# Kernel optimization log

Measured on AMD Instinct MI355X. Metric: run time of the kernel, lower is better.

## Reference

```python
import jax, jax.numpy as jnp
import numpy as np

B = 4      # cfg.TRAIN.IMS_PER_BATCH
P = 256    # proposals per image (equal per image; all labels > 0)
C = 151    # cfg.MODEL.NUM_CLASSES
R = 51     # cfg.MODEL.NUM_RELATIONS
W = 0.5    # cfg.REL_INFER.NONE_BGREL_WEIGHT


def setup_inputs() -> dict:
    key = jax.random.key(0)
    k1, k2, k3, k4 = jax.random.split(key, 4)
    roi_scores = jax.random.normal(k1, (B * P, C), dtype=jnp.float32)
    rel_scores = jax.random.normal(k2, (B * P * P, R), dtype=jnp.float32)
    roi_labels = jax.random.randint(k3, (B * P,), 1, C, dtype=jnp.int32)  # labels > 0 (fg only)
    # sparse relation co-occurrence matrix densified; background relation slice set to 1
    relationship_mat = (jax.random.uniform(k4, (C, C, R)) < 0.05).astype(jnp.float32)
    relationship_mat = relationship_mat.at[:, :, 0].set(1.0)
    return {
        "roi_scores": roi_scores,
        "rel_scores": rel_scores,
        "relationship_mat": relationship_mat,
        "roi_labels": roi_labels,
        "num_images": B,
    }


def reference(roi_scores, rel_scores, relationship_mat, roi_labels, num_images):
    nb = num_images
    p = roi_scores.shape[0] // nb
    rel = rel_scores.reshape(nb, p, p, -1)          # [B, P, P, R]
    labels = roi_labels.reshape(nb, p)              # [B, P]
    # computed in the original forward but unused by the returned loss
    _unary = jax.nn.log_softmax(roi_scores, axis=1)
    off_diag = (1.0 - jnp.eye(p, dtype=roi_scores.dtype))  # zero out p == q pairs

    def per_image(lab, rl):
        # lab: [P] int, rl: [P, P, R]
        A = relationship_mat[lab]        # [P, C, R]  rows gathered by subject label
        At = relationship_mat[:, lab]    # [C, P, R]  cols gathered by subject label
        # b[p,q,c] = A[p,c,0]*rl[p,q,0] + W * sum_{r>=1} A[p,c,r]*rl[p,q,r]
        b = A[:, None, :, 0] * rl[:, :, None, 0] \
            + W * jnp.einsum('pcr,pqr->pqc', A[..., 1:], rl[..., 1:])
        # t[p,q,c] = At[c,p,0]*rl[q,p,0] + W * sum_{r>=1} At[c,p,r]*rl[q,p,r]
        t = At[..., 0].T[:, None, :] * rl[..., 0].T[:, :, None] \
            + W * jnp.einsum('cpr,qpr->pqc', At[..., 1:], rl[..., 1:])
        theta = 0.5 * (b + t) * off_diag[:, :, None]  # mask diagonal pairs
        theta = theta.sum(0)                          # sum over partner p -> [P, C]
        logp = jax.nn.log_softmax(theta, axis=1)
        return -logp[jnp.arange(p), lab]              # [P]

    loss = jax.vmap(per_image)(labels, rel)           # [B, P]
    return loss.mean()
```

## Files before the change

### kernel.cpp

```cpp
#include <hip/hip_runtime.h>
#include <math.h>

#define NB 4
#define PP 256
#define CC 151
#define RR 51
#define CM 160
#define KI 64
#define KS 64
#define NROW (NB*PP)
#define RELTOT (NB*PP*PP*RR)
#define ALIM (RELTOT - 8)
#define MLB 10240

typedef _Float16 half8 __attribute__((ext_vector_type(8)));
typedef float floatx16 __attribute__((ext_vector_type(16)));

#define OFF_M1 ((size_t)0)
#define OFF_M2 (OFF_M1 + (size_t)CC*MLB*2)
#define OFF_PT (OFF_M2 + (size_t)CC*MLB*2)

__global__ __launch_bounds__(256) void prep_kernel(const float* __restrict__ M,
                                                   _Float16* __restrict__ m1,
                                                   _Float16* __restrict__ m2,
                                                   float* __restrict__ out) {
    const int l = blockIdx.x;
    const int mat = blockIdx.y;
    if (l == 0 && mat == 0 && threadIdx.x == 0) *out = 0.f;
    _Float16* dst = (mat ? m2 : m1) + (size_t)l * MLB;
    for (int e = threadIdx.x; e < MLB; e += 256) {
        int oct = e / 1280;
        int rem = e - oct * 1280;
        int c = rem >> 3, j = rem & 7;
        int r = oct * 8 + j;
        float v = 0.f;
        if (r < RR && c < CC) {
            size_t src = ((size_t)(mat ? c * CC + l : l * CC + c)) * RR + r;
            v = (r == 0 ? 0.5f : 0.25f) * M[src];
        }
        dst[e] = (_Float16)v;
    }
}

__global__ __launch_bounds__(256) void gemm_kernel(const float* __restrict__ rel,
                                                   const _Float16* __restrict__ m1,
                                                   const _Float16* __restrict__ m2,
                                                   const int* __restrict__ labels,
                                                   float* __restrict__ part) {
    __shared__ _Float16 Bt[2][2560];
    const int tid  = threadIdx.x;
    const int ks   = blockIdx.x & 63;
    const int rbk  = (blockIdx.x >> 6) & 1;
    const int n    = blockIdx.x >> 7;
    const int wave = tid >> 6, lane = tid & 63;
    const int m32  = lane & 31, kh = lane >> 5;
    const int i0   = ks * 4;
    const int rowimg = rbk * 128 + wave * 32 + m32;

    int labs[4];
    #pragma unroll
    for (int j = 0; j < 4; ++j) labs[j] = labels[n * PP + i0 + j];

    floatx16 acc[5];
    #pragma unroll
    for (int ct = 0; ct < 5; ++ct)
        #pragma unroll
        for (int r2 = 0; r2 < 16; ++r2) acc[ct][r2] = 0.f;

    auto stageB = [&](int h, int buf) {
        const int il = h >> 3, mh = (h >> 2) & 1, t = h & 3;
        const _Float16* base = (mh ? m2 : m1) + (size_t)labs[il] * MLB + t * 2560;
        #pragma unroll
        for (int j = 0; j < 2; ++j) {
            int s = j * 256 + tid;
            if (s < 320) {
                __builtin_amdgcn_global_load_lds(
                    (const __attribute__((address_space(1))) unsigned int*)(base + s * 8),
                    (__attribute__((address_space(3))) unsigned int*)(&Bt[buf][(size_t)s * 8]),
                    16, 0, 0);
            }
        }
    };
    auto loadA = [&](int h, float* v) {
        const int il = h >> 3, mh = (h >> 2) & 1, t = h & 3;
        const int i = i0 + il;
        const int r0 = t * 16 + kh * 8;
        int idx = mh ? ((n * PP + rowimg) * PP + i) * RR + r0
                     : ((n * PP + i) * PP + rowimg) * RR + r0;
        idx = min(idx, ALIM);
        const float* p = rel + idx;
        #pragma unroll
        for (int j = 0; j < 8; ++j) v[j] = p[j];
    };

    stageB(0, 0);
    float av[8];
    loadA(0, av);

    #pragma unroll 2
    for (int h = 0; h < 32; ++h) {
        __syncthreads();
        if (h < 31) stageB(h + 1, (h + 1) & 1);
        float avn[8];
        if (h < 31) loadA(h + 1, avn);

        const bool dz = (i0 + (h >> 3)) == rowimg;
        half8 a;
        #pragma unroll
        for (int j = 0; j < 8; ++j) a[j] = (_Float16)(dz ? 0.f : av[j]);

        const _Float16* bb = &Bt[h & 1][(size_t)(kh * 160 + m32) * 8];
        #pragma unroll
        for (int ct = 0; ct < 5; ++ct) {
            half8 b = *(const half8*)(bb + ct * 256);
            acc[ct] = __builtin_amdgcn_mfma_f32_32x32x16_f16(a, b, acc[ct], 0, 0, 0);
        }
        #pragma unroll
        for (int j = 0; j < 8; ++j) av[j] = avn[j];
    }

    float* pb = part + ((size_t)ks * NROW + n * PP + rbk * 128 + wave * 32) * CM;
    #pragma unroll
    for (int ct = 0; ct < 5; ++ct)
        #pragma unroll
        for (int reg = 0; reg < 16; ++reg) {
            int row = (reg & 3) + 8 * (reg >> 2) + 4 * kh;
            pb[(size_t)row * CM + ct * 32 + m32] = acc[ct][reg];
        }
}

__global__ __launch_bounds__(256) void reduce_loss_kernel(const float* __restrict__ part,
                                                          const int* __restrict__ labels,
                                                          float* __restrict__ out) {
    __shared__ float th[CM];
    const int row = blockIdx.x;
    const int t = threadIdx.x;
    if (t < CM) {
        float s = 0.f;
        #pragma unroll
        for (int ks = 0; ks < KS; ++ks)
            s += part[((size_t)ks * NROW + row) * CM + t];
        th[t] = s;
    }
    __syncthreads();
    if (t < 64) {
        float v0 = (t < CC)       ? th[t]       : -INFINITY;
        float v1 = (t + 64 < CC)  ? th[t + 64]  : -INFINITY;
        float v2 = (t + 128 < CC) ? th[t + 128] : -INFINITY;
        float m = fmaxf(v0, fmaxf(v1, v2));
        #pragma unroll
        for (int o = 32; o > 0; o >>= 1) m = fmaxf(m, __shfl_xor(m, o, 64));
        float s = 0.f;
        if (t < CC)       s += expf(v0 - m);
        if (t + 64 < CC)  s += expf(v1 - m);
        if (t + 128 < CC) s += expf(v2 - m);
        #pragma unroll
        for (int o = 32; o > 0; o >>= 1) s += __shfl_xor(s, o, 64);
        if (t == 0) {
            atomicAdd(out, (m + logf(s) - th[labels[row]]) * (1.0f / NROW));
        }
    }
}

extern "C" void kernel_launch(void* const* d_in, const int* in_sizes, int n_in,
                              void* d_out, int out_size, void* d_ws, size_t ws_size,
                              hipStream_t stream) {
    const float* rel    = (const float*)d_in[1];
    const float* relmat = (const float*)d_in[2];
    const int*   labels = (const int*)d_in[3];
    float* out = (float*)d_out;
    char* ws = (char*)d_ws;

    _Float16* m1 = (_Float16*)(ws + OFF_M1);
    _Float16* m2 = (_Float16*)(ws + OFF_M2);
    float*  part = (float*)(ws + OFF_PT);

    prep_kernel<<<dim3(CC, 2), 256, 0, stream>>>(relmat, m1, m2, out);
    gemm_kernel<<<NB * 2 * KS, 256, 0, stream>>>(rel, m1, m2, labels, part);
    reduce_loss_kernel<<<NROW, 256, 0, stream>>>(part, labels, out);
}
```

Baseline: 166.6 us.

## Stage rel tiles through LDS with async loads and 4-deep pipeline

The A operand (rel scores) is now loaded with global_load_lds directly into a swizzled LDS buffer instead of into registers. The B operand staging is reorganized to two loads per thread. Both go into a 4-buffer ring with two steps of prefetch, gated by manual vmcnt waits and barriers. This aims to hide global load latency behind the MFMA work and cut register pressure. The cost is many 4-byte async loads per step and fragile hand-counted waitcnt values.

```diff
diff --git a/kernel.cpp b/kernel.cpp
--- a/kernel.cpp
+++ b/kernel.cpp
@@ -6,15 +6,14 @@
 #define CC 151
 #define RR 51
 #define CM 160
-#define KI 64
 #define KS 64
 #define NROW (NB*PP)
 #define RELTOT (NB*PP*PP*RR)
-#define ALIM (RELTOT - 8)
 #define MLB 10240
 
 typedef _Float16 half8 __attribute__((ext_vector_type(8)));
 typedef float floatx16 __attribute__((ext_vector_type(16)));
+typedef float float4v __attribute__((ext_vector_type(4)));
 
 #define OFF_M1 ((size_t)0)
 #define OFF_M2 (OFF_M1 + (size_t)CC*MLB*2)
@@ -47,7 +46,8 @@
                                                    const _Float16* __restrict__ m2,
                                                    const int* __restrict__ labels,
                                                    float* __restrict__ part) {
-    __shared__ _Float16 Bt[2][2560];
+    __shared__ float    ldsA[4][2048];
+    __shared__ _Float16 ldsB[4][2560];
     const int tid  = threadIdx.x;
     const int ks   = blockIdx.x & 63;
     const int rbk  = (blockIdx.x >> 6) & 1;
@@ -55,11 +55,18 @@
     const int wave = tid >> 6, lane = tid & 63;
     const int m32  = lane & 31, kh = lane >> 5;
     const int i0   = ks * 4;
-    const int rowimg = rbk * 128 + wave * 32 + m32;
+    const int row_loc = wave * 32 + m32;
+    const int rowimg  = rbk * 128 + row_loc;
 
-    int labs[4];
-    #pragma unroll
-    for (int j = 0; j < 4; ++j) labs[j] = labels[n * PP + i0 + j];
+    const int l0 = labels[n * PP + i0 + 0];
+    const int l1 = labels[n * PP + i0 + 1];
+    const int l2 = labels[n * PP + i0 + 2];
+    const int l3 = labels[n * PP + i0 + 3];
+
+    const int s_swz = (row_loc >> 1) & 3;
+    const int pA    = (2 * kh) ^ s_swz;
+    const int aoffL = row_loc * 16 + pA * 4;
+    const int aoffH = row_loc * 16 + (pA ^ 1) * 4;
 
     floatx16 acc[5];
     #pragma unroll
@@ -67,56 +74,67 @@
         #pragma unroll
         for (int r2 = 0; r2 < 16; ++r2) acc[ct][r2] = 0.f;
 
-    auto stageB = [&](int h, int buf) {
+    auto issueStep = [&](int h, int buf) {
         const int il = h >> 3, mh = (h >> 2) & 1, t = h & 3;
-        const _Float16* base = (mh ? m2 : m1) + (size_t)labs[il] * MLB + t * 2560;
+        const int i = i0 + il;
+        const int lab = (il & 2) ? ((il & 1) ? l3 : l2) : ((il & 1) ? l1 : l0);
+        const _Float16* mb = (mh ? m2 : m1) + (size_t)lab * MLB + t * 2560;
+        __builtin_amdgcn_global_load_lds(
+            (const __attribute__((address_space(1))) unsigned int*)(mb + tid * 8),
+            (__attribute__((address_space(3))) unsigned int*)(&ldsB[buf][tid * 8]),
+            16, 0, 0);
+        __builtin_amdgcn_global_load_lds(
+            (const __attribute__((address_space(1))) unsigned int*)(mb + 2048 + tid * 2),
+            (__attribute__((address_space(3))) unsigned int*)(&ldsB[buf][2048 + tid * 2]),
+            4, 0, 0);
         #pragma unroll
-        for (int j = 0; j < 2; ++j) {
-            int s = j * 256 + tid;
-            if (s < 320) {
-                __builtin_amdgcn_global_load_lds(
-                    (const __attribute__((address_space(1))) unsigned int*)(base + s * 8),
-                    (__attribute__((address_space(3))) unsigned int*)(&Bt[buf][(size_t)s * 8]),
-                    16, 0, 0);
-            }
+        for (int jj = 0; jj < 8; ++jj) {
+            const int tau = jj * 256 + tid;
+            const int row = tau >> 4;
+            const int q   = (tau >> 2) & 3;
+            const int e   = tau & 3;
+            const int ql  = q ^ ((row >> 1) & 3);
+            const int rg  = rbk * 128 + row;
+            int f = (mh ? ((n * PP + rg) * PP + i)
+                        : ((n * PP + i) * PP + rg)) * RR + t * 16 + ql * 4 + e;
+            f = min(f, RELTOT - 1);
+            __builtin_amdgcn_global_load_lds(
+                (const __attribute__((address_space(1))) unsigned int*)(rel + f),
+                (__attribute__((address_space(3))) unsigned int*)(&ldsA[buf][tau]),
+                4, 0, 0);
         }
     };
-    auto loadA = [&](int h, float* v) {
-        const int il = h >> 3, mh = (h >> 2) & 1, t = h & 3;
-        const int i = i0 + il;
-        const int r0 = t * 16 + kh * 8;
-        int idx = mh ? ((n * PP + rowimg) * PP + i) * RR + r0
-                     : ((n * PP + i) * PP + rowimg) * RR + r0;
-        idx = min(idx, ALIM);
-        const float* p = rel + idx;
-        #pragma unroll
-        for (int j = 0; j < 8; ++j) v[j] = p[j];
-    };
 
-    stageB(0, 0);
-    float av[8];
-    loadA(0, av);
-
-    #pragma unroll 2
-    for (int h = 0; h < 32; ++h) {
-        __syncthreads();
-        if (h < 31) stageB(h + 1, (h + 1) & 1);
-        float avn[8];
-        if (h < 31) loadA(h + 1, avn);
-
-        const bool dz = (i0 + (h >> 3)) == rowimg;
+    auto computeStep = [&](int h, int buf) {
+        const int il = h >> 3;
+        const bool dz = (i0 + il) == rowimg;
+        const float4v alo = *(const float4v*)(&ldsA[buf][aoffL]);
+        const float4v ahi = *(const float4v*)(&ldsA[buf][aoffH]);
         half8 a;
         #pragma unroll
-        for (int j = 0; j < 8; ++j) a[j] = (_Float16)(dz ? 0.f : av[j]);
-
-        const _Float16* bb = &Bt[h & 1][(size_t)(kh * 160 + m32) * 8];
+        for (int j = 0; j < 4; ++j) {
+            a[j]     = (_Float16)(dz ? 0.f : alo[j]);
+            a[j + 4] = (_Float16)(dz ? 0.f : ahi[j]);
+        }
+        const _Float16* bb = &ldsB[buf][(kh * 160 + m32) * 8];
         #pragma unroll
         for (int ct = 0; ct < 5; ++ct) {
             half8 b = *(const half8*)(bb + ct * 256);
             acc[ct] = __builtin_amdgcn_mfma_f32_32x32x16_f16(a, b, acc[ct], 0, 0, 0);
         }
-        #pragma unroll
-        for (int j = 0; j < 8; ++j) av[j] = avn[j];
+    };
+
+    issueStep(0, 0);
+    issueStep(1, 1);
+
+    for (int h = 0; h < 32; ++h) {
+        if (h < 30) issueStep(h + 2, (h + 2) & 3);
+        if (h < 30)       asm volatile("s_waitcnt vmcnt(20)" ::: "memory");
+        else if (h == 30) asm volatile("s_waitcnt vmcnt(10)" ::: "memory");
+        else              asm volatile("s_waitcnt vmcnt(0)"  ::: "memory");
+        __builtin_amdgcn_s_barrier();
+        asm volatile("" ::: "memory");
+        computeStep(h, h & 3);
     }
 
     float* pb = part + ((size_t)ks * NROW + n * PP + rbk * 128 + wave * 32) * CM;
```

Result: slower. 232.5 us (+39.5%).

## Load B operand directly into registers and drop LDS staging and barriers

Applied to the files above, without the earlier changes.

The GEMM kernel no longer stages the relation-matrix tile into shared memory through global_load_lds with a barrier each step. Each lane now loads its B fragments straight from global memory into registers, using a fully unrolled two-deep register double buffer for both A and B. Launch bounds now request two blocks per SM. This removes the per-step __syncthreads and the LDS round trip, but each wave issues its own redundant B loads and register pressure rises.

```diff
diff --git a/kernel.cpp b/kernel.cpp
--- a/kernel.cpp
+++ b/kernel.cpp
@@ -6,7 +6,6 @@
 #define CC 151
 #define RR 51
 #define CM 160
-#define KI 64
 #define KS 64
 #define NROW (NB*PP)
 #define RELTOT (NB*PP*PP*RR)
@@ -42,12 +41,11 @@
     }
 }
 
-__global__ __launch_bounds__(256) void gemm_kernel(const float* __restrict__ rel,
-                                                   const _Float16* __restrict__ m1,
-                                                   const _Float16* __restrict__ m2,
-                                                   const int* __restrict__ labels,
-                                                   float* __restrict__ part) {
-    __shared__ _Float16 Bt[2][2560];
+__global__ __launch_bounds__(256, 2) void gemm_kernel(const float* __restrict__ rel,
+                                                      const _Float16* __restrict__ m1,
+                                                      const _Float16* __restrict__ m2,
+                                                      const int* __restrict__ labels,
+                                                      float* __restrict__ part) {
     const int tid  = threadIdx.x;
     const int ks   = blockIdx.x & 63;
     const int rbk  = (blockIdx.x >> 6) & 1;
@@ -67,20 +65,6 @@
         #pragma unroll
         for (int r2 = 0; r2 < 16; ++r2) acc[ct][r2] = 0.f;
 
-    auto stageB = [&](int h, int buf) {
-        const int il = h >> 3, mh = (h >> 2) & 1, t = h & 3;
-        const _Float16* base = (mh ? m2 : m1) + (size_t)labs[il] * MLB + t * 2560;
-        #pragma unroll
-        for (int j = 0; j < 2; ++j) {
-            int s = j * 256 + tid;
-            if (s < 320) {
-                __builtin_amdgcn_global_load_lds(
-                    (const __attribute__((address_space(1))) unsigned int*)(base + s * 8),
-                    (__attribute__((address_space(3))) unsigned int*)(&Bt[buf][(size_t)s * 8]),
-                    16, 0, 0);
-            }
-        }
-    };
     auto loadA = [&](int h, float* v) {
         const int il = h >> 3, mh = (h >> 2) & 1, t = h & 3;
         const int i = i0 + il;
@@ -92,31 +76,35 @@
         #pragma unroll
         for (int j = 0; j < 8; ++j) v[j] = p[j];
     };
-
-    stageB(0, 0);
-    float av[8];
-    loadA(0, av);
-
-    #pragma unroll 2
-    for (int h = 0; h < 32; ++h) {
-        __syncthreads();
-        if (h < 31) stageB(h + 1, (h + 1) & 1);
-        float avn[8];
-        if (h < 31) loadA(h + 1, avn);
-
-        const bool dz = (i0 + (h >> 3)) == rowimg;
+    auto loadB = [&](int h, half8* b) {
+        const int il = h >> 3, mh = (h >> 2) & 1, t = h & 3;
+        const _Float16* p = (mh ? m2 : m1) + (size_t)labs[il] * MLB + t * 2560
+                          + (size_t)(kh * 160 + m32) * 8;
+        #pragma unroll
+        for (int ct = 0; ct < 5; ++ct) b[ct] = *(const half8*)(p + ct * 256);
+    };
+    auto computeStep = [&](int h, const float* av, const half8* bv) {
+        const int il = h >> 3;
+        const bool dz = (i0 + il) == rowimg;
         half8 a;
         #pragma unroll
         for (int j = 0; j < 8; ++j) a[j] = (_Float16)(dz ? 0.f : av[j]);
+        #pragma unroll
+        for (int ct = 0; ct < 5; ++ct)
+            acc[ct] = __builtin_amdgcn_mfma_f32_32x32x16_f16(a, bv[ct], acc[ct], 0, 0, 0);
+    };
 
-        const _Float16* bb = &Bt[h & 1][(size_t)(kh * 160 + m32) * 8];
-        #pragma unroll
-        for (int ct = 0; ct < 5; ++ct) {
-            half8 b = *(const half8*)(bb + ct * 256);
-            acc[ct] = __builtin_amdgcn_mfma_f32_32x32x16_f16(a, b, acc[ct], 0, 0, 0);
-        }
-        #pragma unroll
-        for (int j = 0; j < 8; ++j) av[j] = avn[j];
+    float aA[8], aB[8];
+    half8 bA[5], bB[5];
+    loadA(0, aA); loadB(0, bA);
+    loadA(1, aB); loadB(1, bB);
+
+    #pragma unroll
+    for (int h = 0; h < 32; h += 2) {
+        computeStep(h, aA, bA);
+        if (h + 2 < 32) { loadA(h + 2, aA); loadB(h + 2, bA); }
+        computeStep(h + 1, aB, bB);
+        if (h + 3 < 32) { loadA(h + 3, aB); loadB(h + 3, bB); }
     }
 
     float* pb = part + ((size_t)ks * NROW + n * PP + rbk * 128 + wave * 32) * CM;
```

Measured after the change: 173.1 us. 3.9% more time.

## Pre-convert relation scores to padded fp16 rows with diagonal zeroed

Applied to the files above, without the earlier changes.

Adds a pass inside the prep kernel that converts the fp32 relation-score tensor into fp16 rows padded to 64 entries, zeroing diagonal pairs and the padding. The GEMM kernel then loads eight halves per lane with one aligned vector load, instead of eight scalar fp32 loads followed by conversion and a diagonal check. This swaps strided unaligned fp32 reads in the GEMM for one extra full pass over the ~53MB rel tensor plus a ~33MB fp16 write, which may cost more bandwidth than it saves.

```diff
diff --git a/kernel.cpp b/kernel.cpp
--- a/kernel.cpp
+++ b/kernel.cpp
@@ -6,43 +6,65 @@
 #define CC 151
 #define RR 51
 #define CM 160
-#define KI 64
 #define KS 64
 #define NROW (NB*PP)
-#define RELTOT (NB*PP*PP*RR)
-#define ALIM (RELTOT - 8)
 #define MLB 10240
+#define NRELROW (NB*PP*PP)
+#define CONVB (NRELROW/8)
+#define PREPB (CC*2)
 
 typedef _Float16 half8 __attribute__((ext_vector_type(8)));
+typedef _Float16 half2v __attribute__((ext_vector_type(2)));
 typedef float floatx16 __attribute__((ext_vector_type(16)));
 
 #define OFF_M1 ((size_t)0)
 #define OFF_M2 (OFF_M1 + (size_t)CC*MLB*2)
 #define OFF_PT (OFF_M2 + (size_t)CC*MLB*2)
+#define OFF_R16 (OFF_PT + (size_t)KS*NROW*CM*4)
 
 __global__ __launch_bounds__(256) void prep_kernel(const float* __restrict__ M,
+                                                   const float* __restrict__ rel,
                                                    _Float16* __restrict__ m1,
                                                    _Float16* __restrict__ m2,
+                                                   _Float16* __restrict__ rel16,
                                                    float* __restrict__ out) {
-    const int l = blockIdx.x;
-    const int mat = blockIdx.y;
-    if (l == 0 && mat == 0 && threadIdx.x == 0) *out = 0.f;
-    _Float16* dst = (mat ? m2 : m1) + (size_t)l * MLB;
-    for (int e = threadIdx.x; e < MLB; e += 256) {
-        int oct = e / 1280;
-        int rem = e - oct * 1280;
-        int c = rem >> 3, j = rem & 7;
-        int r = oct * 8 + j;
-        float v = 0.f;
-        if (r < RR && c < CC) {
-            size_t src = ((size_t)(mat ? c * CC + l : l * CC + c)) * RR + r;
-            v = (r == 0 ? 0.5f : 0.25f) * M[src];
+    const int bid = blockIdx.x;
+    if (bid < PREPB) {
+        const int l = (bid < CC) ? bid : bid - CC;
+        const int mat = (bid < CC) ? 0 : 1;
+        if (bid == 0 && threadIdx.x == 0) *out = 0.f;
+        _Float16* dst = (mat ? m2 : m1) + (size_t)l * MLB;
+        for (int e = threadIdx.x; e < MLB; e += 256) {
+            int oct = e / 1280;
+            int rem = e - oct * 1280;
+            int c = rem >> 3, j = rem & 7;
+            int r = oct * 8 + j;
+            float v = 0.f;
+            if (r < RR && c < CC) {
+                size_t src = ((size_t)(mat ? c * CC + l : l * CC + c)) * RR + r;
+                v = (r == 0 ? 0.5f : 0.25f) * M[src];
+            }
+            dst[e] = (_Float16)v;
         }
-        dst[e] = (_Float16)v;
+    } else {
+        const int t = threadIdx.x;
+        const size_t row = (size_t)(bid - PREPB) * 8 + (t >> 5);
+        const int d  = t & 31;
+        const int h0 = 2 * d;
+        const int a  = ((int)row >> 8) & 255;
+        const int b  = (int)row & 255;
+        const bool live = (a != b);
+        const float* src = rel + row * RR;
+        float v0 = (live && h0 < RR)     ? src[h0]     : 0.f;
+        float v1 = (live && h0 + 1 < RR) ? src[h0 + 1] : 0.f;
+        half2v p;
+        p[0] = (_Float16)v0;
+        p[1] = (_Float16)v1;
+        *(half2v*)(rel16 + row * 64 + h0) = p;
     }
 }
 
-__global__ __launch_bounds__(256) void gemm_kernel(const float* __restrict__ rel,
+__global__ __launch_bounds__(256) void gemm_kernel(const _Float16* __restrict__ rel16,
                                                    const _Float16* __restrict__ m1,
                                                    const _Float16* __restrict__ m2,
                                                    const int* __restrict__ labels,
@@ -81,42 +103,32 @@
             }
         }
     };
-    auto loadA = [&](int h, float* v) {
+    auto loadA = [&](int h, half8* a) {
         const int il = h >> 3, mh = (h >> 2) & 1, t = h & 3;
         const int i = i0 + il;
-        const int r0 = t * 16 + kh * 8;
-        int idx = mh ? ((n * PP + rowimg) * PP + i) * RR + r0
-                     : ((n * PP + i) * PP + rowimg) * RR + r0;
-        idx = min(idx, ALIM);
-        const float* p = rel + idx;
-        #pragma unroll
-        for (int j = 0; j < 8; ++j) v[j] = p[j];
+        const size_t row = mh ? ((size_t)(n * PP + rowimg) * PP + i)
+                              : ((size_t)(n * PP + i) * PP + rowimg);
+        *a = *(const half8*)(rel16 + row * 64 + t * 16 + kh * 8);
     };
 
     stageB(0, 0);
-    float av[8];
-    loadA(0, av);
+    half8 av;
+    loadA(0, &av);
 
     #pragma unroll 2
     for (int h = 0; h < 32; ++h) {
         __syncthreads();
         if (h < 31) stageB(h + 1, (h + 1) & 1);
-        float avn[8];
-        if (h < 31) loadA(h + 1, avn);
-
-        const bool dz = (i0 + (h >> 3)) == rowimg;
-        half8 a;
-        #pragma unroll
-        for (int j = 0; j < 8; ++j) a[j] = (_Float16)(dz ? 0.f : av[j]);
+        half8 avn;
+        if (h < 31) loadA(h + 1, &avn);
 
         const _Float16* bb = &Bt[h & 1][(size_t)(kh * 160 + m32) * 8];
         #pragma unroll
         for (int ct = 0; ct < 5; ++ct) {
             half8 b = *(const half8*)(bb + ct * 256);
-            acc[ct] = __builtin_amdgcn_mfma_f32_32x32x16_f16(a, b, acc[ct], 0, 0, 0);
+            acc[ct] = __builtin_amdgcn_mfma_f32_32x32x16_f16(av, b, acc[ct], 0, 0, 0);
         }
-        #pragma unroll
-        for (int j = 0; j < 8; ++j) av[j] = avn[j];
+        av = avn;
     }
 
     float* pb = part + ((size_t)ks * NROW + n * PP + rbk * 128 + wave * 32) * CM;
@@ -171,11 +183,12 @@
     float* out = (float*)d_out;
     char* ws = (char*)d_ws;
 
-    _Float16* m1 = (_Float16*)(ws + OFF_M1);
-    _Float16* m2 = (_Float16*)(ws + OFF_M2);
-    float*  part = (float*)(ws + OFF_PT);
+    _Float16* m1    = (_Float16*)(ws + OFF_M1);
+    _Float16* m2    = (_Float16*)(ws + OFF_M2);
+    float*    part  = (float*)(ws + OFF_PT);
+    _Float16* rel16 = (_Float16*)(ws + OFF_R16);
 
-    prep_kernel<<<dim3(CC, 2), 256, 0, stream>>>(relmat, m1, m2, out);
-    gemm_kernel<<<NB * 2 * KS, 256, 0, stream>>>(rel, m1, m2, labels, part);
+    prep_kernel<<<PREPB + CONVB, 256, 0, stream>>>(relmat, rel, m1, m2, rel16, out);
+    gemm_kernel<<<NB * 2 * KS, 256, 0, stream>>>(rel16, m1, m2, labels, part);
     reduce_loss_kernel<<<NROW, 256, 0, stream>>>(part, labels, out);
 }
```

Result: no change. 166.3 us (-0.2%).
